# Kernel optimization log

Hardware: AMD Instinct MI355X
Metric: run time of the kernel (lower is better)

Reference implementation:

```python
import jax, jax.numpy as jnp
import numpy as np

D = 384      # pct_dim == spm_dim == d_model
H = 6        # heads
DK = D // H  # 64
HID = 96     # int(384 * 0.25)
B = 8
NS = 2040    # multiple of 85 (SPM pyramid 64+16+4+1 groups)
NP = 2048


def _ln(x, g, b, eps):
    m = x.mean(-1, keepdims=True)
    v = jnp.mean((x - m) ** 2, -1, keepdims=True)
    return (x - m) * jax.lax.rsqrt(v + eps) * g + b


def setup_inputs() -> dict:
    key = jax.random.key(0)
    ks = jax.random.split(key, 10)
    w = lambda k, shape: jax.random.normal(k, shape, jnp.float32) * 0.02
    p = {
        "spm_feature": jax.random.normal(ks[0], (B, NS, D), jnp.float32),
        "pct_feature": jax.random.normal(ks[1], (B, NP, D), jnp.float32),
        # extractor pre-norms (eps=1e-6)
        "pct_g": jnp.ones(D), "pct_b": jnp.zeros(D),
        "spm_g": jnp.ones(D), "spm_b": jnp.zeros(D),
        # CrossAttention internal norms (eps=1e-5)
        "lnx_g": jnp.ones(D), "lnx_b": jnp.zeros(D),
        "lny_g": jnp.ones(D), "lny_b": jnp.zeros(D),
        "Wq": w(ks[2], (D, D)), "bq": jnp.zeros(D),
        "Wk": w(ks[3], (D, D)), "bk": jnp.zeros(D),
        "Wv": w(ks[4], (D, D)), "bv": jnp.zeros(D),
        # 1x1 Conv1d in CrossAttention
        "Wc": w(ks[5], (D, D)), "bc": jnp.zeros(D),
        "lnc_g": jnp.ones(D), "lnc_b": jnp.zeros(D),
        # FFN
        "ffn_g": jnp.ones(D), "ffn_b": jnp.zeros(D),
        "W1": w(ks[6], (HID, D)), "b1": jnp.zeros(HID),
        "Wdw": w(ks[7], (HID, HID)), "bdw": jnp.zeros(HID),
        "W2": w(ks[8], (D, HID)), "b2": jnp.zeros(D),
    }
    return p


def reference(spm_feature, pct_feature, pct_g, pct_b, spm_g, spm_b,
              lnx_g, lnx_b, lny_g, lny_b, Wq, bq, Wk, bk, Wv, bv,
              Wc, bc, lnc_g, lnc_b, ffn_g, ffn_b, W1, b1, Wdw, bdw, W2, b2):
    EPS6, EPS5 = 1e-6, 1e-5
    # extractor pre-norms (the (N,B,C) permutes in the torch code cancel for LN)
    x = _ln(spm_feature, spm_g, spm_b, EPS6)
    y = _ln(pct_feature, pct_g, pct_b, EPS6)
    # CrossAttention's own (double) LayerNorms
    xn = _ln(x, lnx_g, lnx_b, EPS5)
    yn = _ln(y, lny_g, lny_b, EPS5)
    Bq, Nq, _ = xn.shape
    q = (xn @ Wq.T + bq).reshape(Bq, Nq, H, DK)
    k = (yn @ Wk.T + bk).reshape(Bq, -1, H, DK)
    v = (yn @ Wv.T + bv).reshape(Bq, -1, H, DK)
    scale = 1.0 / np.sqrt(DK).astype(np.float32)
    scores = jnp.einsum('bqhd,bkhd->bhqk', q, k) * scale
    att = jax.nn.softmax(scores, axis=-1)
    # non-standard extra renormalization across the HEAD dimension (dim=1)
    att = att / (1e-9 + att.sum(axis=1, keepdims=True))
    o = jnp.einsum('bhqk,bkhd->bqhd', att, v).reshape(Bq, Nq, D)
    qf = q.reshape(Bq, Nq, D)
    r = (qf - o) @ Wc.T + bc            # 1x1 Conv1d == channel linear
    r = _ln(r, lnc_g, lnc_b, EPS5)
    r = jnp.where(r > 0, r, 0.02 * r)    # LeakyReLU(0.02)
    cross = qf + r
    spm = spm_feature + cross            # first residual
    # FFN: fc1 -> (4-way segment split, shared 1x1 dwconv1, concat) -> gelu -> fc2
    # a 1x1 Conv1d with shared weights applied to contiguous segments then
    # concatenated is mathematically identical to one application on the full seq
    h = _ln(spm, ffn_g, ffn_b, EPS5)
    h = h @ W1.T + b1                    # (B, NS, 96)
    h = h @ Wdw.T + bdw                  # shared 1x1 conv over channels
    h = jax.nn.gelu(h, approximate=False)
    h = h @ W2.T + b2                    # (B, NS, 384)
    return spm + h
```

## Files before the change

### kernel.cpp

```cpp
#include <hip/hip_runtime.h>
#include <hip/hip_bf16.h>
#include <math.h>

#define D 384
#define NHEAD 6
#define DKH 64
#define HID 96
#define BB 8
#define NS 2040
#define NPK 2048

typedef __attribute__((ext_vector_type(8))) short short8;
typedef __attribute__((ext_vector_type(4))) float f32x4;

__device__ __forceinline__ float bf2f(ushort u) {
  union { uint u; float f; } x; x.u = ((uint)u) << 16; return x.f;
}
__device__ __forceinline__ ushort f2bf(float f) {
  union { float f; uint u; } x; x.f = f;
  uint r = x.u + 0x7fffu + ((x.u >> 16) & 1u);
  return (ushort)(r >> 16);
}
__device__ __forceinline__ float ldin(const void* p, size_t i, bool f32) {
  return f32 ? ((const float*)p)[i] : bf2f(((const ushort*)p)[i]);
}
__device__ __forceinline__ uint4 load8bf(const void* p, size_t off, bool f32) {
  if (!f32) return *(const uint4*)((const ushort*)p + off);
  const float* f = (const float*)p + off;
  float4 a = *(const float4*)f, b = *(const float4*)(f + 4);
  uint4 r;
  r.x = (uint)f2bf(a.x) | ((uint)f2bf(a.y) << 16);
  r.y = (uint)f2bf(a.z) | ((uint)f2bf(a.w) << 16);
  r.z = (uint)f2bf(b.x) | ((uint)f2bf(b.y) << 16);
  r.w = (uint)f2bf(b.z) | ((uint)f2bf(b.w) << 16);
  return r;
}
__device__ __forceinline__ uint bfsub2(uint a, uint b) {
  float lo = bf2f((ushort)(a & 0xffffu)) - bf2f((ushort)(b & 0xffffu));
  float hi = bf2f((ushort)(a >> 16))     - bf2f((ushort)(b >> 16));
  return (uint)f2bf(lo) | ((uint)f2bf(hi) << 16);
}

__global__ void probe_dtype(const void* ones_vec, int* flg) {
  if (threadIdx.x == 0 && blockIdx.x == 0) {
    uint u = *(const uint*)ones_vec;
    *flg = (u == 0x3F800000u) ? 1 : 0;
  }
}

__global__ __launch_bounds__(256) void ln2_kernel(
    const void* __restrict__ src,
    const void* __restrict__ g1, const void* __restrict__ b1,
    const void* __restrict__ g2, const void* __restrict__ b2,
    ushort* __restrict__ dst, const int* __restrict__ flg,
    int rows, float eps1, float eps2)
{
  const bool f32 = *flg != 0;
  int row = blockIdx.x * 4 + (threadIdx.x >> 6);
  int lane = threadIdx.x & 63;
  if (row >= rows) return;
  float v[6];
#pragma unroll
  for (int j = 0; j < 3; ++j) {
    int c = 2 * (lane + 64 * j);
    v[2*j]   = ldin(src, (size_t)row * D + c,     f32);
    v[2*j+1] = ldin(src, (size_t)row * D + c + 1, f32);
  }
  float s = 0.f, s2 = 0.f;
#pragma unroll
  for (int i = 0; i < 6; ++i) { s += v[i]; s2 += v[i]*v[i]; }
#pragma unroll
  for (int off = 32; off; off >>= 1) { s += __shfl_xor(s, off); s2 += __shfl_xor(s2, off); }
  float mean = s * (1.f/D);
  float rstd = rsqrtf(fmaxf(s2*(1.f/D) - mean*mean, 0.f) + eps1);
  float t[6];
  float u = 0.f, u2 = 0.f;
#pragma unroll
  for (int j = 0; j < 3; ++j) {
    int c = 2 * (lane + 64 * j);
#pragma unroll
    for (int i = 0; i < 2; ++i) {
      float val = (v[2*j+i] - mean) * rstd * ldin(g1, c+i, f32) + ldin(b1, c+i, f32);
      t[2*j+i] = val; u += val; u2 += val*val;
    }
  }
#pragma unroll
  for (int off = 32; off; off >>= 1) { u += __shfl_xor(u, off); u2 += __shfl_xor(u2, off); }
  float mean2 = u * (1.f/D);
  float rstd2 = rsqrtf(fmaxf(u2*(1.f/D) - mean2*mean2, 0.f) + eps2);
  ushort* q = dst + (size_t)row * D;
#pragma unroll
  for (int j = 0; j < 3; ++j) {
    int c = 2 * (lane + 64 * j);
    ushort lo = f2bf((t[2*j]   - mean2) * rstd2 * ldin(g2, c,   f32) + ldin(b2, c,   f32));
    ushort hi = f2bf((t[2*j+1] - mean2) * rstd2 * ldin(g2, c+1, f32) + ldin(b2, c+1, f32));
    *(uint*)(q + c) = (uint)lo | ((uint)hi << 16);
  }
}

template<int EPI, int ASUB>
__global__ __launch_bounds__(256) void gemm_bt(
    const ushort* __restrict__ A, const ushort* __restrict__ A2,
    const void* __restrict__ W, const void* __restrict__ bias,
    const ushort* __restrict__ resid, void* __restrict__ Cout,
    const int* __restrict__ flg, int M, int N, int K)
{
  const bool f32 = *flg != 0;
  __shared__ ushort As[64][40];
  __shared__ ushort Ws[64][40];
  int tm = blockIdx.x * 64, tn = blockIdx.y * 64;
  int tid = threadIdx.x;
  int wv = tid >> 6, lane = tid & 63;
  f32x4 acc[4] = {{0,0,0,0},{0,0,0,0},{0,0,0,0},{0,0,0,0}};
  int lrow = tid >> 2, lc8 = (tid & 3) * 8;
  for (int k0 = 0; k0 < K; k0 += 32) {
    __syncthreads();
    uint4 aval = *(const uint4*)(A + (size_t)(tm + lrow) * K + k0 + lc8);
    if (ASUB) {
      uint4 bval = *(const uint4*)(A2 + (size_t)(tm + lrow) * K + k0 + lc8);
      aval.x = bfsub2(aval.x, bval.x); aval.y = bfsub2(aval.y, bval.y);
      aval.z = bfsub2(aval.z, bval.z); aval.w = bfsub2(aval.w, bval.w);
    }
    *(uint4*)&As[lrow][lc8] = aval;
    uint4 wval = make_uint4(0,0,0,0);
    int wr = tn + lrow;
    if (wr < N) wval = load8bf(W, (size_t)wr * K + k0 + lc8, f32);
    *(uint4*)&Ws[lrow][lc8] = wval;
    __syncthreads();
    short8 af = *(const short8*)&As[16*wv + (lane & 15)][8*(lane >> 4)];
#pragma unroll
    for (int n = 0; n < 4; ++n) {
      short8 bfr = *(const short8*)&Ws[16*n + (lane & 15)][8*(lane >> 4)];
      acc[n] = __builtin_amdgcn_mfma_f32_16x16x32_bf16(af, bfr, acc[n], 0, 0, 0);
    }
  }
  int rbase = tm + 16*wv + 4*(lane >> 4);
#pragma unroll
  for (int n = 0; n < 4; ++n) {
    int col = tn + 16*n + (lane & 15);
    if (col >= N) continue;
    float bv = ldin(bias, col, f32);
#pragma unroll
    for (int e = 0; e < 4; ++e) {
      int row = rbase + e;
      float val = acc[n][e] + bv;
      if (EPI == 1) val = 0.5f * val * (1.f + erff(val * 0.70710678118654752f));
      if (EPI == 2) val += bf2f(resid[(size_t)row * N + col]);
      if (EPI == 2 && f32) {
        ((float*)Cout)[(size_t)row * N + col] = val;
      } else {
        ((ushort*)Cout)[(size_t)row * N + col] = f2bf(val);
      }
    }
  }
}

__global__ __launch_bounds__(256) void vt_tr(
    const ushort* __restrict__ v, ushort* __restrict__ vt)
{
  __shared__ ushort T[64][66];
  int k0 = blockIdx.x * 64, d0 = blockIdx.y * 64, b = blockIdx.z;
  int tid = threadIdx.x;
#pragma unroll
  for (int i = 0; i < 2; ++i) {
    int f = tid + 256*i;
    int r = f >> 3, c8 = (f & 7) * 8;
    uint4 w = *(const uint4*)(v + (size_t)(b*NPK + k0 + r)*D + d0 + c8);
    const ushort* wsp = (const ushort*)&w;
#pragma unroll
    for (int j = 0; j < 8; ++j) T[r][c8 + j] = wsp[j];
  }
  __syncthreads();
#pragma unroll
  for (int i = 0; i < 2; ++i) {
    int f = tid + 256*i;
    int r = f >> 3, c8 = (f & 7) * 8;
    ushort tmp[8];
#pragma unroll
    for (int j = 0; j < 8; ++j) tmp[j] = T[c8 + j][r];
    *(uint4*)(vt + (size_t)(b*D + d0 + r)*NPK + k0 + c8) = *(const uint4*)tmp;
  }
}

__global__ __launch_bounds__(256) void attn_mz(
    const ushort* __restrict__ q, const ushort* __restrict__ k,
    float* __restrict__ mmout)
{
  __shared__ ushort Ksh[64][72];
  int qt = blockIdx.x, h = blockIdx.y, b = blockIdx.z;
  int tid = threadIdx.x, wv = tid >> 6, lane = tid & 63;
  int l15 = lane & 15, l4 = lane >> 4;
  int q0 = qt*64 + wv*16;
  const float C = 0.18033688011112042f;
  int qrow = q0 + l15; if (qrow > NS-1) qrow = NS-1;
  const ushort* qp = q + (size_t)(b*NS + qrow)*D + h*64 + l4*8;
  short8 qf0 = *(const short8*)(qp);
  short8 qf1 = *(const short8*)(qp + 32);
  float m[4] = {-1e30f,-1e30f,-1e30f,-1e30f};
  float z[4] = {0.f,0.f,0.f,0.f};
  for (int kt = 0; kt < NPK; kt += 64) {
    __syncthreads();
#pragma unroll
    for (int i = 0; i < 2; ++i) {
      int f = tid + 256*i;
      int r = f >> 3, c8 = (f & 7) * 8;
      *(uint4*)&Ksh[r][c8] = *(const uint4*)(k + (size_t)(b*NPK + kt + r)*D + h*64 + c8);
    }
    __syncthreads();
#pragma unroll
    for (int ks = 0; ks < 4; ++ks) {
      short8 b0 = *(const short8*)&Ksh[ks*16 + l15][l4*8];
      short8 b1 = *(const short8*)&Ksh[ks*16 + l15][32 + l4*8];
      f32x4 t = {0.f,0.f,0.f,0.f};
      t = __builtin_amdgcn_mfma_f32_16x16x32_bf16(qf0, b0, t, 0, 0, 0);
      t = __builtin_amdgcn_mfma_f32_16x16x32_bf16(qf1, b1, t, 0, 0, 0);
#pragma unroll
      for (int e = 0; e < 4; ++e) {
        float u = t[e] * C;
        float mn = fmaxf(m[e], u);
        z[e] = z[e]*exp2f(m[e]-mn) + exp2f(u-mn);
        m[e] = mn;
      }
    }
  }
#pragma unroll
  for (int off = 1; off < 16; off <<= 1) {
#pragma unroll
    for (int e = 0; e < 4; ++e) {
      float mo = __shfl_xor(m[e], off);
      float zo = __shfl_xor(z[e], off);
      float mn = fmaxf(m[e], mo);
      z[e] = z[e]*exp2f(m[e]-mn) + zo*exp2f(mo-mn);
      m[e] = mn;
    }
  }
  if (l15 == 0) {
#pragma unroll
    for (int e = 0; e < 4; ++e) {
      int row = q0 + l4*4 + e;
      if (row < NS) mmout[(size_t)(b*NHEAD + h)*NS + row] = m[e] + log2f(z[e]);
    }
  }
}

__global__ __launch_bounds__(256, 1) void attn_pv(
    const ushort* __restrict__ q, const ushort* __restrict__ k,
    const ushort* __restrict__ vt, const float* __restrict__ mm,
    ushort* __restrict__ o)
{
  __shared__ ushort Ks[64][392];
  __shared__ ushort Vt[384][72];
  __shared__ ushort Wl[4][16][72];
  int qt = blockIdx.x, b = blockIdx.y;
  int tid = threadIdx.x, wv = tid >> 6, lane = tid & 63;
  int l15 = lane & 15, l4 = lane >> 4;
  int q0 = qt*64 + wv*16;
  const float C = 0.18033688011112042f;
  int qrow = q0 + l15; if (qrow > NS-1) qrow = NS-1;
  short8 qf[12];
#pragma unroll
  for (int c = 0; c < 12; ++c)
    qf[c] = *(const short8*)(q + (size_t)(b*NS + qrow)*D + c*32 + l4*8);
  float mmr[6][4];
#pragma unroll
  for (int h = 0; h < 6; ++h)
#pragma unroll
    for (int e = 0; e < 4; ++e) {
      int row = q0 + l4*4 + e; if (row > NS-1) row = NS-1;
      mmr[h][e] = mm[(size_t)(b*NHEAD + h)*NS + row];
    }
  f32x4 acc[6][4];
#pragma unroll
  for (int h = 0; h < 6; ++h)
#pragma unroll
    for (int n = 0; n < 4; ++n) acc[h][n] = f32x4{0.f,0.f,0.f,0.f};

  for (int kt = 0; kt < NPK; kt += 64) {
    __syncthreads();
#pragma unroll
    for (int i = 0; i < 12; ++i) {
      int f = tid + 256*i;
      int r = f / 48, c = (f % 48) * 8;
      *(uint4*)&Ks[r][c] = *(const uint4*)(k + (size_t)(b*NPK + kt + r)*D + c);
    }
#pragma unroll
    for (int i = 0; i < 12; ++i) {
      int f = tid + 256*i;
      int r = f >> 3, c8 = (f & 7) * 8;
      *(uint4*)&Vt[r][c8] = *(const uint4*)(vt + (size_t)(b*D + r)*NPK + kt + c8);
    }
    __syncthreads();
    f32x4 s[6][4];
#pragma unroll
    for (int h = 0; h < 6; ++h)
#pragma unroll
      for (int ks = 0; ks < 4; ++ks) {
        short8 b0 = *(const short8*)&Ks[ks*16 + l15][h*64 + l4*8];
        short8 b1 = *(const short8*)&Ks[ks*16 + l15][h*64 + 32 + l4*8];
        f32x4 t = {0.f,0.f,0.f,0.f};
        t = __builtin_amdgcn_mfma_f32_16x16x32_bf16(qf[2*h],   b0, t, 0, 0, 0);
        t = __builtin_amdgcn_mfma_f32_16x16x32_bf16(qf[2*h+1], b1, t, 0, 0, 0);
        s[h][ks] = t;
      }
#pragma unroll
    for (int ks = 0; ks < 4; ++ks)
#pragma unroll
      for (int e = 0; e < 4; ++e) {
        float w6[6];
        float sum = 1e-9f;
#pragma unroll
        for (int h = 0; h < 6; ++h) {
          w6[h] = exp2f(s[h][ks][e]*C - mmr[h][e]);
          sum += w6[h];
        }
        float inv = __builtin_amdgcn_rcpf(sum);
#pragma unroll
        for (int h = 0; h < 6; ++h) s[h][ks][e] = w6[h]*inv;
      }
#pragma unroll
    for (int h = 0; h < 6; ++h) {
#pragma unroll
      for (int ks = 0; ks < 4; ++ks)
#pragma unroll
        for (int e = 0; e < 4; ++e)
          Wl[wv][l4*4 + e][ks*16 + l15] = f2bf(s[h][ks][e]);
      short8 a0 = *(const short8*)&Wl[wv][l15][l4*8];
      short8 a1 = *(const short8*)&Wl[wv][l15][32 + l4*8];
#pragma unroll
      for (int n = 0; n < 4; ++n) {
        short8 v0 = *(const short8*)&Vt[h*64 + 16*n + l15][l4*8];
        short8 v1 = *(const short8*)&Vt[h*64 + 16*n + l15][32 + l4*8];
        acc[h][n] = __builtin_amdgcn_mfma_f32_16x16x32_bf16(a0, v0, acc[h][n], 0, 0, 0);
        acc[h][n] = __builtin_amdgcn_mfma_f32_16x16x32_bf16(a1, v1, acc[h][n], 0, 0, 0);
      }
    }
  }
#pragma unroll
  for (int h = 0; h < 6; ++h)
#pragma unroll
    for (int n = 0; n < 4; ++n)
#pragma unroll
      for (int e = 0; e < 4; ++e) {
        int row = q0 + l4*4 + e;
        if (row < NS) o[(size_t)(b*NS + row)*D + h*64 + 16*n + l15] = f2bf(acc[h][n][e]);
      }
}

__global__ __launch_bounds__(256) void cross_kernel(
    const ushort* __restrict__ rtmp, const ushort* __restrict__ q,
    const void* __restrict__ spm,
    const void* __restrict__ lg, const void* __restrict__ lb,
    ushort* __restrict__ spm2, const int* __restrict__ flg, int rows)
{
  const bool f32 = *flg != 0;
  int row = blockIdx.x * 4 + (threadIdx.x >> 6);
  int lane = threadIdx.x & 63;
  if (row >= rows) return;
  const ushort* rp = rtmp + (size_t)row * D;
  float v[6];
#pragma unroll
  for (int j = 0; j < 3; ++j) {
    uint w = *(const uint*)(rp + 2*(lane + 64*j));
    v[2*j]   = bf2f((ushort)(w & 0xffffu));
    v[2*j+1] = bf2f((ushort)(w >> 16));
  }
  float s = 0.f, s2 = 0.f;
#pragma unroll
  for (int i = 0; i < 6; ++i) { s += v[i]; s2 += v[i]*v[i]; }
#pragma unroll
  for (int off = 32; off; off >>= 1) { s += __shfl_xor(s, off); s2 += __shfl_xor(s2, off); }
  float mean = s * (1.f/D);
  float rstd = rsqrtf(fmaxf(s2*(1.f/D) - mean*mean, 0.f) + 1e-5f);
  const ushort* qp = q + (size_t)row * D;
  ushort* op = spm2 + (size_t)row * D;
#pragma unroll
  for (int j = 0; j < 3; ++j) {
    int c = 2*(lane + 64*j);
#pragma unroll
    for (int i = 0; i < 2; ++i) {
      float r = (v[2*j+i] - mean)*rstd*ldin(lg, c+i, f32) + ldin(lb, c+i, f32);
      r = r > 0.f ? r : 0.02f*r;
      float ov = ldin(spm, (size_t)row*D + c + i, f32) + bf2f(qp[c+i]) + r;
      op[c+i] = f2bf(ov);
    }
  }
}

__global__ __launch_bounds__(256) void ln_bf16(
    const ushort* __restrict__ src, const void* __restrict__ g,
    const void* __restrict__ b, ushort* __restrict__ dst,
    const int* __restrict__ flg, int rows, float eps)
{
  const bool f32 = *flg != 0;
  int row = blockIdx.x * 4 + (threadIdx.x >> 6);
  int lane = threadIdx.x & 63;
  if (row >= rows) return;
  const ushort* p = src + (size_t)row * D;
  float v[6];
#pragma unroll
  for (int j = 0; j < 3; ++j) {
    uint w = *(const uint*)(p + 2*(lane + 64*j));
    v[2*j]   = bf2f((ushort)(w & 0xffffu));
    v[2*j+1] = bf2f((ushort)(w >> 16));
  }
  float s = 0.f, s2 = 0.f;
#pragma unroll
  for (int i = 0; i < 6; ++i) { s += v[i]; s2 += v[i]*v[i]; }
#pragma unroll
  for (int off = 32; off; off >>= 1) { s += __shfl_xor(s, off); s2 += __shfl_xor(s2, off); }
  float mean = s * (1.f/D);
  float rstd = rsqrtf(fmaxf(s2*(1.f/D) - mean*mean, 0.f) + eps);
  ushort* o = dst + (size_t)row * D;
#pragma unroll
  for (int j = 0; j < 3; ++j) {
    int c = 2*(lane + 64*j);
    ushort lo = f2bf((v[2*j]   - mean)*rstd*ldin(g, c,   f32) + ldin(b, c,   f32));
    ushort hi = f2bf((v[2*j+1] - mean)*rstd*ldin(g, c+1, f32) + ldin(b, c+1, f32));
    *(uint*)(o + c) = (uint)lo | ((uint)hi << 16);
  }
}

extern "C" void kernel_launch(void* const* d_in, const int* in_sizes, int n_in,
                              void* d_out, int out_size, void* d_ws, size_t ws_size,
                              hipStream_t stream)
{
  const void* spm   = d_in[0];
  const void* pct   = d_in[1];
  const void* pct_g = d_in[2];
  const void* pct_b = d_in[3];
  const void* spm_g = d_in[4];
  const void* spm_b = d_in[5];
  const void* lnx_g = d_in[6];
  const void* lnx_b = d_in[7];
  const void* lny_g = d_in[8];
  const void* lny_b = d_in[9];
  const void* Wq = d_in[10]; const void* bq = d_in[11];
  const void* Wk = d_in[12]; const void* bk = d_in[13];
  const void* Wv = d_in[14]; const void* bv = d_in[15];
  const void* Wc = d_in[16]; const void* bc = d_in[17];
  const void* lnc_g = d_in[18]; const void* lnc_b = d_in[19];
  const void* ffn_g = d_in[20]; const void* ffn_b = d_in[21];
  const void* W1 = d_in[22];  const void* b1 = d_in[23];
  const void* Wdw = d_in[24]; const void* bdw = d_in[25];
  const void* W2 = d_in[26];  const void* b2 = d_in[27];

  char* ws = (char*)d_ws;
  int*    flg  = (int*)(ws + 0);
  ushort* kb   = (ushort*)(ws + 256);
  ushort* vb   = (ushort*)(ws + 12583168);
  ushort* qb   = (ushort*)(ws + 25166080);
  ushort* vtg  = (ushort*)(ws + 37699840);
  char*   R    = ws + 50282752;
  ushort* xn   = (ushort*)R;
  ushort* yn   = (ushort*)R;
  ushort* ob   = (ushort*)R;
  float*  mmb  = (float*)(R + 12533760);
  ushort* rtmp = vb;
  ushort* spm2 = kb;
  ushort* hin  = qb;
  ushort* h1   = (ushort*)R;
  ushort* h2   = (ushort*)(R + 3133440);

  const int M_S = BB * NS;
  const int M_P = BB * NPK;

  probe_dtype<<<1, 64, 0, stream>>>(pct_g, flg);
  ln2_kernel<<<M_S/4, 256, 0, stream>>>(spm, spm_g, spm_b, lnx_g, lnx_b, xn, flg, M_S, 1e-6f, 1e-5f);
  gemm_bt<0,0><<<dim3(M_S/64, 6), 256, 0, stream>>>(xn, nullptr, Wq, bq, nullptr, qb, flg, M_S, D, D);
  ln2_kernel<<<M_P/4, 256, 0, stream>>>(pct, pct_g, pct_b, lny_g, lny_b, yn, flg, M_P, 1e-6f, 1e-5f);
  gemm_bt<0,0><<<dim3(M_P/64, 6), 256, 0, stream>>>(yn, nullptr, Wk, bk, nullptr, kb, flg, M_P, D, D);
  gemm_bt<0,0><<<dim3(M_P/64, 6), 256, 0, stream>>>(yn, nullptr, Wv, bv, nullptr, vb, flg, M_P, D, D);
  vt_tr<<<dim3(NPK/64, D/64, BB), 256, 0, stream>>>(vb, vtg);
  attn_mz<<<dim3(32, NHEAD, BB), 256, 0, stream>>>(qb, kb, mmb);
  attn_pv<<<dim3(32, BB), 256, 0, stream>>>(qb, kb, vtg, mmb, ob);
  gemm_bt<0,1><<<dim3(M_S/64, 6), 256, 0, stream>>>(qb, ob, Wc, bc, nullptr, rtmp, flg, M_S, D, D);
  cross_kernel<<<M_S/4, 256, 0, stream>>>(rtmp, qb, spm, lnc_g, lnc_b, spm2, flg, M_S);
  ln_bf16<<<M_S/4, 256, 0, stream>>>(spm2, ffn_g, ffn_b, hin, flg, M_S, 1e-5f);
  gemm_bt<0,0><<<dim3(M_S/64, 2), 256, 0, stream>>>(hin, nullptr, W1, b1, nullptr, h1, flg, M_S, HID, D);
  gemm_bt<1,0><<<dim3(M_S/64, 2), 256, 0, stream>>>(h1, nullptr, Wdw, bdw, nullptr, h2, flg, M_S, HID, HID);
  gemm_bt<2,0><<<dim3(M_S/64, 6), 256, 0, stream>>>(h2, nullptr, W2, b2, spm2, d_out, flg, M_S, D, HID);
}
```

Measured before the change: 565.6 us.

## Shrink attn_pv key tile, raise occupancy, and fuse cross with FFN layernorm

```diff
diff --git a/kernel.cpp b/kernel.cpp
--- a/kernel.cpp
+++ b/kernel.cpp
@@ -243,14 +243,14 @@
   }
 }
 
-__global__ __launch_bounds__(256, 1) void attn_pv(
+__global__ __launch_bounds__(256, 2) void attn_pv(
     const ushort* __restrict__ q, const ushort* __restrict__ k,
     const ushort* __restrict__ vt, const float* __restrict__ mm,
     ushort* __restrict__ o)
 {
-  __shared__ ushort Ks[64][392];
-  __shared__ ushort Vt[384][72];
-  __shared__ ushort Wl[4][16][72];
+  __shared__ ushort Ks[32][392];
+  __shared__ ushort Vt[384][40];
+  __shared__ ushort Wl[4][16][40];
   int qt = blockIdx.x, b = blockIdx.y;
   int tid = threadIdx.x, wv = tid >> 6, lane = tid & 63;
   int l15 = lane & 15, l4 = lane >> 4;
@@ -269,32 +269,34 @@
       int row = q0 + l4*4 + e; if (row > NS-1) row = NS-1;
       mmr[h][e] = mm[(size_t)(b*NHEAD + h)*NS + row];
     }
+  int prr = (l15 & 1) + 2*(l15 >> 2) + 8*((l15 >> 1) & 1);
   f32x4 acc[6][4];
 #pragma unroll
   for (int h = 0; h < 6; ++h)
 #pragma unroll
     for (int n = 0; n < 4; ++n) acc[h][n] = f32x4{0.f,0.f,0.f,0.f};
 
-  for (int kt = 0; kt < NPK; kt += 64) {
-    __syncthreads();
-#pragma unroll
-    for (int i = 0; i < 12; ++i) {
+  for (int kt = 0; kt < NPK; kt += 32) {
+    __syncthreads();
+#pragma unroll
+    for (int i = 0; i < 6; ++i) {
       int f = tid + 256*i;
       int r = f / 48, c = (f % 48) * 8;
       *(uint4*)&Ks[r][c] = *(const uint4*)(k + (size_t)(b*NPK + kt + r)*D + c);
     }
 #pragma unroll
-    for (int i = 0; i < 12; ++i) {
+    for (int i = 0; i < 6; ++i) {
       int f = tid + 256*i;
-      int r = f >> 3, c8 = (f & 7) * 8;
+      int r = f >> 2, c8 = (f & 3) * 8;
       *(uint4*)&Vt[r][c8] = *(const uint4*)(vt + (size_t)(b*D + r)*NPK + kt + c8);
     }
     __syncthreads();
-    f32x4 s[6][4];
+    f32x4 s[6][2];
+    __builtin_amdgcn_s_setprio(1);
 #pragma unroll
     for (int h = 0; h < 6; ++h)
 #pragma unroll
-      for (int ks = 0; ks < 4; ++ks) {
+      for (int ks = 0; ks < 2; ++ks) {
         short8 b0 = *(const short8*)&Ks[ks*16 + l15][h*64 + l4*8];
         short8 b1 = *(const short8*)&Ks[ks*16 + l15][h*64 + 32 + l4*8];
         f32x4 t = {0.f,0.f,0.f,0.f};
@@ -302,8 +304,9 @@
         t = __builtin_amdgcn_mfma_f32_16x16x32_bf16(qf[2*h+1], b1, t, 0, 0, 0);
         s[h][ks] = t;
       }
-#pragma unroll
-    for (int ks = 0; ks < 4; ++ks)
+    __builtin_amdgcn_s_setprio(0);
+#pragma unroll
+    for (int ks = 0; ks < 2; ++ks)
 #pragma unroll
       for (int e = 0; e < 4; ++e) {
         float w6[6];
@@ -320,19 +323,18 @@
 #pragma unroll
     for (int h = 0; h < 6; ++h) {
 #pragma unroll
-      for (int ks = 0; ks < 4; ++ks)
+      for (int ks = 0; ks < 2; ++ks)
 #pragma unroll
         for (int e = 0; e < 4; ++e)
-          Wl[wv][l4*4 + e][ks*16 + l15] = f2bf(s[h][ks][e]);
-      short8 a0 = *(const short8*)&Wl[wv][l15][l4*8];
-      short8 a1 = *(const short8*)&Wl[wv][l15][32 + l4*8];
+          Wl[wv][(e & 1) + 2*l4 + 8*(e >> 1)][ks*16 + l15] = f2bf(s[h][ks][e]);
+      short8 a0 = *(const short8*)&Wl[wv][prr][l4*8];
+      __builtin_amdgcn_s_setprio(1);
 #pragma unroll
       for (int n = 0; n < 4; ++n) {
         short8 v0 = *(const short8*)&Vt[h*64 + 16*n + l15][l4*8];
-        short8 v1 = *(const short8*)&Vt[h*64 + 16*n + l15][32 + l4*8];
         acc[h][n] = __builtin_amdgcn_mfma_f32_16x16x32_bf16(a0, v0, acc[h][n], 0, 0, 0);
-        acc[h][n] = __builtin_amdgcn_mfma_f32_16x16x32_bf16(a1, v1, acc[h][n], 0, 0, 0);
-      }
+      }
+      __builtin_amdgcn_s_setprio(0);
     }
   }
 #pragma unroll
@@ -346,11 +348,13 @@
       }
 }
 
-__global__ __launch_bounds__(256) void cross_kernel(
+__global__ __launch_bounds__(256) void cross_ln(
     const ushort* __restrict__ rtmp, const ushort* __restrict__ q,
     const void* __restrict__ spm,
     const void* __restrict__ lg, const void* __restrict__ lb,
-    ushort* __restrict__ spm2, const int* __restrict__ flg, int rows)
+    const void* __restrict__ fg, const void* __restrict__ fb,
+    ushort* __restrict__ spm2, ushort* __restrict__ hin,
+    const int* __restrict__ flg, int rows)
 {
   const bool f32 = *flg != 0;
   int row = blockIdx.x * 4 + (threadIdx.x >> 6);
@@ -373,6 +377,8 @@
   float rstd = rsqrtf(fmaxf(s2*(1.f/D) - mean*mean, 0.f) + 1e-5f);
   const ushort* qp = q + (size_t)row * D;
   ushort* op = spm2 + (size_t)row * D;
+  float t[6];
+  float u = 0.f, u2 = 0.f;
 #pragma unroll
   for (int j = 0; j < 3; ++j) {
     int c = 2*(lane + 64*j);
@@ -382,41 +388,20 @@
       r = r > 0.f ? r : 0.02f*r;
       float ov = ldin(spm, (size_t)row*D + c + i, f32) + bf2f(qp[c+i]) + r;
       op[c+i] = f2bf(ov);
-    }
-  }
-}
-
-__global__ __launch_bounds__(256) void ln_bf16(
-    const ushort* __restrict__ src, const void* __restrict__ g,
-    const void* __restrict__ b, ushort* __restrict__ dst,
-    const int* __restrict__ flg, int rows, float eps)
-{
-  const bool f32 = *flg != 0;
-  int row = blockIdx.x * 4 + (threadIdx.x >> 6);
-  int lane = threadIdx.x & 63;
-  if (row >= rows) return;
-  const ushort* p = src + (size_t)row * D;
-  float v[6];
-#pragma unroll
-  for (int j = 0; j < 3; ++j) {
-    uint w = *(const uint*)(p + 2*(lane + 64*j));
-    v[2*j]   = bf2f((ushort)(w & 0xffffu));
-    v[2*j+1] = bf2f((ushort)(w >> 16));
-  }
-  float s = 0.f, s2 = 0.f;
-#pragma unroll
-  for (int i = 0; i < 6; ++i) { s += v[i]; s2 += v[i]*v[i]; }
-#pragma unroll
-  for (int off = 32; off; off >>= 1) { s += __shfl_xor(s, off); s2 += __shfl_xor(s2, off); }
-  float mean = s * (1.f/D);
-  float rstd = rsqrtf(fmaxf(s2*(1.f/D) - mean*mean, 0.f) + eps);
-  ushort* o = dst + (size_t)row * D;
+      t[2*j+i] = ov; u += ov; u2 += ov*ov;
+    }
+  }
+#pragma unroll
+  for (int off = 32; off; off >>= 1) { u += __shfl_xor(u, off); u2 += __shfl_xor(u2, off); }
+  float mean2 = u * (1.f/D);
+  float rstd2 = rsqrtf(fmaxf(u2*(1.f/D) - mean2*mean2, 0.f) + 1e-5f);
+  ushort* hp = hin + (size_t)row * D;
 #pragma unroll
   for (int j = 0; j < 3; ++j) {
     int c = 2*(lane + 64*j);
-    ushort lo = f2bf((v[2*j]   - mean)*rstd*ldin(g, c,   f32) + ldin(b, c,   f32));
-    ushort hi = f2bf((v[2*j+1] - mean)*rstd*ldin(g, c+1, f32) + ldin(b, c+1, f32));
-    *(uint*)(o + c) = (uint)lo | ((uint)hi << 16);
+    ushort lo = f2bf((t[2*j]   - mean2)*rstd2*ldin(fg, c,   f32) + ldin(fb, c,   f32));
+    ushort hi = f2bf((t[2*j+1] - mean2)*rstd2*ldin(fg, c+1, f32) + ldin(fb, c+1, f32));
+    *(uint*)(hp + c) = (uint)lo | ((uint)hi << 16);
   }
 }
 
@@ -474,8 +459,7 @@
   attn_mz<<<dim3(32, NHEAD, BB), 256, 0, stream>>>(qb, kb, mmb);
   attn_pv<<<dim3(32, BB), 256, 0, stream>>>(qb, kb, vtg, mmb, ob);
   gemm_bt<0,1><<<dim3(M_S/64, 6), 256, 0, stream>>>(qb, ob, Wc, bc, nullptr, rtmp, flg, M_S, D, D);
-  cross_kernel<<<M_S/4, 256, 0, stream>>>(rtmp, qb, spm, lnc_g, lnc_b, spm2, flg, M_S);
-  ln_bf16<<<M_S/4, 256, 0, stream>>>(spm2, ffn_g, ffn_b, hin, flg, M_S, 1e-5f);
+  cross_ln<<<M_S/4, 256, 0, stream>>>(rtmp, qb, spm, lnc_g, lnc_b, ffn_g, ffn_b, spm2, hin, flg, M_S);
   gemm_bt<0,0><<<dim3(M_S/64, 2), 256, 0, stream>>>(hin, nullptr, W1, b1, nullptr, h1, flg, M_S, HID, D);
   gemm_bt<1,0><<<dim3(M_S/64, 2), 256, 0, stream>>>(h1, nullptr, Wdw, bdw, nullptr, h2, flg, M_S, HID, HID);
   gemm_bt<2,0><<<dim3(M_S/64, 6), 256, 0, stream>>>(h2, nullptr, W2, b2, spm2, d_out, flg, M_S, D, HID);
```

Result: slower. 705.6 us (+24.8%).
